# Kernel optimization log

Hardware: AMD Instinct MI355X
Metric: run time of the kernel (lower is better)

The kernel has to match this reference:

```python
import jax, jax.numpy as jnp
import numpy as np

B, S, D, H = 2, 1024, 1024, 16
DK, DV = 64, 64
E, F, K = 8, 2048, 2
FSH = 2 * F  # n_shared_experts * moe_inter_dim


def layernorm(x, w, eps=1e-8):
    # RMSNormLayer actually calls F.layer_norm(x, [dim], weight, None, eps)
    mu = jnp.mean(x, axis=-1, keepdims=True)
    var = jnp.mean((x - mu) ** 2, axis=-1, keepdims=True)
    return (x - mu) * jax.lax.rsqrt(var + eps) * w


def _forward(start_pos, x, mask, pos_embedding, attn_norm_w, ffn_norm_w,
             wq, bq, wk, bk, wv, bv, wo, bo, gate_w, gate_b,
             ew1, eb1, ew2, eb2, ew3, eb3, sw1, sb1, sw2, sb2, sw3, sb3):
    b, s, d = x.shape
    # --- attention sublayer ---
    xn = layernorm(x, attn_norm_w)
    q = (xn @ wq + bq).reshape(b, s, H, DK)
    k = (xn @ wk + bk).reshape(b, s, H, DK)
    v = (xn @ wv + bv).reshape(b, s, H, DV)
    score = jnp.einsum('bshk,bShk->bhsS', q, k) / np.float32(np.sqrt(DK))
    pe = pos_embedding[:, start_pos:start_pos + s, start_pos:start_pos + s]  # [H,s,s]
    score = score + pe[None, :, :, :] + mask[:s, :s]
    attn = jax.nn.softmax(score, axis=-1)
    o = jnp.einsum('bhsS,bShv->bshv', attn, v).reshape(b, s, H * DV)
    x = x + o @ wo + bo
    # --- MoE sublayer (eval-path math: y[t] = sum_k w[t,k]*expert_{idx[t,k]}(x[t])) ---
    hn = layernorm(x, ffn_norm_w)
    flat = hn.reshape(-1, d)  # [T, D]
    logits = flat @ gate_w.T + gate_b
    scores = jax.nn.softmax(logits, axis=-1)
    topk_w, topk_idx = jax.lax.top_k(scores, K)
    topk_w = topk_w / (jnp.sum(topk_w, axis=-1, keepdims=True) + 1e-20)
    # per-token per-expert combine weight [T, E]
    comb = jnp.sum(jax.nn.one_hot(topk_idx, E, dtype=flat.dtype) * topk_w[..., None], axis=1)
    # all experts densely (small E), SwiGLU per expert
    a = jnp.einsum('td,edf->tef', flat, ew1) + eb1
    g = jnp.einsum('td,edf->tef', flat, ew3) + eb3
    mid = jax.nn.silu(a) * g
    ye = jnp.einsum('tef,efd->ted', mid, ew2) + eb2  # [T, E, D]
    y = jnp.einsum('te,ted->td', comb, ye)
    # shared experts MLP on the normed input
    shared = (jax.nn.silu(flat @ sw1 + sb1) * (flat @ sw3 + sb3)) @ sw2 + sb2
    return x + (y + shared).reshape(b, s, d)


def setup_inputs() -> dict:
    key = jax.random.key(0)
    ks = jax.random.split(key, 16)
    def rn(i, shape, s=0.02):
        return jax.random.normal(ks[i], shape, jnp.float32) * s
    return dict(
        x=rn(0, (B, S, D), 1.0),
        start_pos=0,
        mask=jnp.zeros((S, S), jnp.float32),
        pos_embedding=rn(1, (H, S, S)),
        attn_norm_w=jnp.ones((D,), jnp.float32),
        ffn_norm_w=jnp.ones((D,), jnp.float32),
        wq=rn(2, (D, H * DK)), bq=jnp.zeros((H * DK,), jnp.float32),
        wk=rn(3, (D, H * DK)), bk=jnp.zeros((H * DK,), jnp.float32),
        wv=rn(4, (D, H * DV)), bv=jnp.zeros((H * DV,), jnp.float32),
        wo=rn(5, (H * DV, D)), bo=jnp.zeros((D,), jnp.float32),
        gate_w=rn(6, (E, D), 1.0), gate_b=rn(7, (E,), 1.0),
        ew1=rn(8, (E, D, F)), eb1=jnp.zeros((E, F), jnp.float32),
        ew2=rn(9, (E, F, D)), eb2=jnp.zeros((E, D), jnp.float32),
        ew3=rn(10, (E, D, F)), eb3=jnp.zeros((E, F), jnp.float32),
        sw1=rn(11, (D, FSH)), sb1=jnp.zeros((FSH,), jnp.float32),
        sw2=rn(12, (FSH, D)), sb2=jnp.zeros((D,), jnp.float32),
        sw3=rn(13, (D, FSH)), sb3=jnp.zeros((FSH,), jnp.float32),
    )


def reference(x, start_pos, mask, pos_embedding, attn_norm_w, ffn_norm_w,
              wq, bq, wk, bk, wv, bv, wo, bo, gate_w, gate_b,
              ew1, eb1, ew2, eb2, ew3, eb3, sw1, sb1, sw2, sb2, sw3, sb3):
    return _forward(start_pos, x, mask, pos_embedding, attn_norm_w, ffn_norm_w,
                    wq, bq, wk, bk, wv, bv, wo, bo, gate_w, gate_b,
                    ew1, eb1, ew2, eb2, ew3, eb3, sw1, sb1, sw2, sb2, sw3, sb3)
```

## Files before the change

### kernel.cpp

```cpp
#include <hip/hip_runtime.h>
#include <hip/hip_bf16.h>

#define BB 2
#define SS 1024
#define DD 1024
#define HH 16
#define DKV 64
#define EE 8
#define FF 2048
#define FSH2 4096

typedef __attribute__((ext_vector_type(8))) short bf16x8;
typedef __attribute__((ext_vector_type(4))) float f32x4;

#define EPI_PLAIN 0
#define EPI_SCATTER 2
#define AM_DENSE 0
#define AM_GATHER 1
#define AM_GROUP 2

__device__ inline unsigned pack_bf2(float lo, float hi) {
    __hip_bfloat162 h = __float22bfloat162_rn(float2{lo, hi});
    union { __hip_bfloat162 h2; unsigned u; } c; c.h2 = h; return c.u;
}
__device__ inline unsigned short bf16_1(float x) {
    union { __hip_bfloat16 b; unsigned short u; } c;
    c.b = __float2bfloat16(x); return c.u;
}

#define LOADT(s, k0) {                                                        \
    const float4* ap4 = (const float4*)(Ap + (k0));                           \
    pa##s##_0 = ap4[0]; pa##s##_1 = ap4[1];                                   \
    pa##s##_2 = ap4[2]; pa##s##_3 = ap4[3];                                   \
    const float* wp = Wcol + (size_t)((k0) + kg * 8) * N;                     \
    _Pragma("unroll")                                                         \
    for (int j = 0; j < 8; ++j) pb##s[j] = wp[(size_t)j * N];                 \
}
#define STAGET(s) {                                                           \
    uint4 aw0, aw1;                                                           \
    aw0.x = pack_bf2(pa##s##_0.x, pa##s##_0.y);                               \
    aw0.y = pack_bf2(pa##s##_0.z, pa##s##_0.w);                               \
    aw0.z = pack_bf2(pa##s##_1.x, pa##s##_1.y);                               \
    aw0.w = pack_bf2(pa##s##_1.z, pa##s##_1.w);                               \
    aw1.x = pack_bf2(pa##s##_2.x, pa##s##_2.y);                               \
    aw1.y = pack_bf2(pa##s##_2.z, pa##s##_2.w);                               \
    aw1.z = pack_bf2(pa##s##_3.x, pa##s##_3.y);                               \
    aw1.w = pack_bf2(pa##s##_3.z, pa##s##_3.w);                               \
    *(uint4*)&As[ar * 40 + ac] = aw0;                                         \
    *(uint4*)&As[ar * 40 + ac + 8] = aw1;                                     \
    uint4 bw;                                                                 \
    bw.x = pack_bf2(pb##s[0], pb##s[1]);  bw.y = pack_bf2(pb##s[2], pb##s[3]);\
    bw.z = pack_bf2(pb##s[4], pb##s[5]);  bw.w = pack_bf2(pb##s[6], pb##s[7]);\
    *(uint4*)&Bs[kg * 512 + bn * 8] = bw;                                     \
}
#define MFMAT() {                                                             \
    bf16x8 af[4], bfr[2];                                                     \
    _Pragma("unroll")                                                         \
    for (int m = 0; m < 4; ++m) {                                             \
        int row = wr * 64 + m * 16 + ll;                                      \
        af[m] = *(const bf16x8*)&As[row * 40 + lh * 8];                       \
    }                                                                         \
    _Pragma("unroll")                                                         \
    for (int n = 0; n < 2; ++n) {                                             \
        int col = wc * 32 + n * 16 + ll;                                      \
        bfr[n] = *(const bf16x8*)&Bs[lh * 512 + col * 8];                     \
    }                                                                         \
    _Pragma("unroll")                                                         \
    for (int m = 0; m < 4; ++m)                                               \
        _Pragma("unroll")                                                     \
        for (int n = 0; n < 2; ++n)                                           \
            acc[m][n] = __builtin_amdgcn_mfma_f32_16x16x32_bf16(af[m], bfr[n], acc[m][n], 0, 0, 0); \
}
#define PHASET(s, nx) {                                                       \
    STAGET(s)                                                                 \
    if ((nx) < NT) LOADT(s, (nx) << 5)                                        \
    asm volatile("s_waitcnt lgkmcnt(0)\n\ts_barrier" ::: "memory");           \
    MFMAT()                                                                   \
    asm volatile("s_barrier" ::: "memory");                                   \
}

template<int EPI, int AMODE, int NSEL, int SPLITK>
__global__ __launch_bounds__(256, 2) void mgemm(
    const float* __restrict__ A,
    const float* __restrict__ W0, const float* __restrict__ W1p, const float* __restrict__ W2p,
    const float* __restrict__ b0, const float* __restrict__ b1p, const float* __restrict__ b2p,
    const float* __restrict__ addsrc,
    float* __restrict__ C0, float* __restrict__ C1p, float* __restrict__ C2p,
    int M, int N, int K,
    const int* __restrict__ tok_list, const int* __restrict__ cnt,
    const int* __restrict__ offs, const float* __restrict__ comb,
    const int* __restrict__ idx0, float* __restrict__ y1)
{
    __shared__ __align__(16) unsigned short As[128 * 40];
    __shared__ __align__(16) unsigned short Bs[64 * 32];
    __shared__ int rows_s[128];
    const int t = threadIdx.x;
    const float* W = W0; const float* bias = b0; float* C = C0;
    if (NSEL == 3) {
        if (blockIdx.z == 1) { W = W1p; bias = b1p; C = C1p; }
        else if (blockIdx.z == 2) { W = W2p; bias = b2p; C = C2p; }
    }
    const int e = (AMODE != AM_DENSE) ? blockIdx.z : 0;
    int ne = M, base = 0;
    if (AMODE != AM_DENSE) {
        ne = cnt[e];
        base = offs[e];
        if ((int)blockIdx.y * 128 >= ne) return;
        W += (size_t)e * K * N;
        bias += (size_t)e * N;
    }
    const int m0 = blockIdx.y * 128;
    const int n0 = blockIdx.x * 64;
    if (AMODE == AM_GATHER) {
        if (t < 128) {
            int li = m0 + t; if (li >= ne) li = ne - 1;
            rows_s[t] = tok_list[e * 2048 + li];
        }
        __syncthreads();
    }
    const int ar = t >> 1;
    const int ac = (t & 1) * 16;
    const int bn = t & 63;
    const int kg = t >> 6;
    long arow;
    if (AMODE == AM_DENSE) arow = m0 + ar;
    else if (AMODE == AM_GATHER) arow = rows_s[ar];
    else { int li = m0 + ar; if (li >= ne) li = ne - 1; arow = base + li; }
    const int Kc = (SPLITK > 1) ? (K / SPLITK) : K;
    const size_t koff = (SPLITK > 1) ? (size_t)blockIdx.z * Kc : 0;
    const float* Ap = A + (size_t)arow * K + ac + koff;
    const float* Wcol = W + koff * N + n0 + bn;
    const int l = t & 63, w = t >> 6;
    const int wr = w >> 1, wc = w & 1;
    const int lh = l >> 4, ll = l & 15;
    f32x4 acc[4][2];
#pragma unroll
    for (int i = 0; i < 4; ++i)
#pragma unroll
        for (int j = 0; j < 2; ++j) acc[i][j] = f32x4{0.f, 0.f, 0.f, 0.f};

    const int NT = Kc >> 5;
    float4 pa0_0, pa0_1, pa0_2, pa0_3; float pb0[8];
    float4 pa1_0, pa1_1, pa1_2, pa1_3; float pb1[8];
    float4 pa2_0, pa2_1, pa2_2, pa2_3; float pb2[8];
    float4 pa3_0, pa3_1, pa3_2, pa3_3; float pb3[8];
    LOADT(0, 0)
    LOADT(1, 32)
    LOADT(2, 64)
    LOADT(3, 96)
    for (int it = 0; it < NT; it += 4) {
        PHASET(0, it + 4)
        PHASET(1, it + 5)
        PHASET(2, it + 6)
        PHASET(3, it + 7)
    }

#pragma unroll
    for (int m = 0; m < 4; ++m) {
#pragma unroll
        for (int n = 0; n < 2; ++n) {
            int colg = n0 + wc * 32 + n * 16 + ll;
            float bvv = (SPLITK > 1) ? 0.f : bias[colg];
#pragma unroll
            for (int j = 0; j < 4; ++j) {
                int li = m0 + wr * 64 + m * 16 + lh * 4 + j;
                float v = acc[m][n][j] + bvv;
                if (SPLITK > 1) {
                    C[(size_t)blockIdx.z * M * N + (size_t)li * N + colg] = v;
                } else if (EPI == EPI_PLAIN) {
                    if (AMODE == AM_DENSE) {
                        if (addsrc) v += addsrc[(size_t)li * N + colg];
                        C[(size_t)li * N + colg] = v;
                    } else {
                        if (li < ne) C[(size_t)(base + li) * N + colg] = v;
                    }
                } else {
                    if (li < ne) {
                        int tok = tok_list[e * 2048 + li];
                        float wgt = comb[tok * 8 + e];
                        float* dst = (idx0[tok] == e) ? C : y1;
                        dst[(size_t)tok * N + colg] = wgt * v;
                    }
                }
            }
        }
    }
}

__global__ __launch_bounds__(256, 2) void mgemmF(
    const float* __restrict__ Amid,
    const float* __restrict__ Smid,
    const float* __restrict__ W2r, const float* __restrict__ B2r,
    const float* __restrict__ W2s, const float* __restrict__ B2s,
    float* __restrict__ y0, float* __restrict__ y1, float* __restrict__ sh,
    const int* __restrict__ tok_list, const int* __restrict__ cnt,
    const int* __restrict__ offs, const float* __restrict__ comb,
    const int* __restrict__ idx0)
{
    __shared__ __align__(16) unsigned short As[128 * 40];
    __shared__ __align__(16) unsigned short Bs[64 * 32];
    const int t = threadIdx.x;
    const int z = blockIdx.z;
    const bool sh_mode = (z == 0);
    const int e = sh_mode ? 0 : (z - 1);
    const int N = DD;
    int K, ne, base;
    const float *A, *W, *bias;
    if (sh_mode) {
        K = FSH2; ne = 2048; base = 0;
        A = Smid; W = W2s; bias = B2s;
    } else {
        K = FF;
        ne = cnt[e];
        base = offs[e];
        if ((int)blockIdx.y * 128 >= ne) return;
        A = Amid;
        W = W2r + (size_t)e * K * N;
        bias = B2r + (size_t)e * N;
    }
    const int m0 = blockIdx.y * 128;
    const int n0 = blockIdx.x * 64;
    const int ar = t >> 1;
    const int ac = (t & 1) * 16;
    const int bn = t & 63;
    const int kg = t >> 6;
    long arow;
    if (sh_mode) arow = m0 + ar;
    else { int li = m0 + ar; if (li >= ne) li = ne - 1; arow = base + li; }
    const float* Ap = A + (size_t)arow * K + ac;
    const float* Wcol = W + n0 + bn;
    const int l = t & 63, w = t >> 6;
    const int wr = w >> 1, wc = w & 1;
    const int lh = l >> 4, ll = l & 15;
    f32x4 acc[4][2];
#pragma unroll
    for (int i = 0; i < 4; ++i)
#pragma unroll
        for (int j = 0; j < 2; ++j) acc[i][j] = f32x4{0.f, 0.f, 0.f, 0.f};

    const int NT = K >> 5;
    float4 pa0_0, pa0_1, pa0_2, pa0_3; float pb0[8];
    float4 pa1_0, pa1_1, pa1_2, pa1_3; float pb1[8];
    float4 pa2_0, pa2_1, pa2_2, pa2_3; float pb2[8];
    float4 pa3_0, pa3_1, pa3_2, pa3_3; float pb3[8];
    LOADT(0, 0)
    LOADT(1, 32)
    LOADT(2, 64)
    LOADT(3, 96)
    for (int it = 0; it < NT; it += 4) {
        PHASET(0, it + 4)
        PHASET(1, it + 5)
        PHASET(2, it + 6)
        PHASET(3, it + 7)
    }

#pragma unroll
    for (int m = 0; m < 4; ++m) {
#pragma unroll
        for (int n = 0; n < 2; ++n) {
            int colg = n0 + wc * 32 + n * 16 + ll;
            float bvv = bias[colg];
#pragma unroll
            for (int j = 0; j < 4; ++j) {
                int li = m0 + wr * 64 + m * 16 + lh * 4 + j;
                float v = acc[m][n][j] + bvv;
                if (sh_mode) {
                    sh[(size_t)li * N + colg] = v;
                } else {
                    if (li < ne) {
                        int tok = tok_list[e * 2048 + li];
                        float wgt = comb[tok * 8 + e];
                        float* dst = (idx0[tok] == e) ? y0 : y1;
                        dst[(size_t)tok * N + colg] = wgt * v;
                    }
                }
            }
        }
    }
}

#define LOAD2T(s, k0) {                                                       \
    const float4* ap4 = (const float4*)(Ap + (k0));                           \
    pa##s##_0 = ap4[0]; pa##s##_1 = ap4[1];                                   \
    pa##s##_2 = ap4[2]; pa##s##_3 = ap4[3];                                   \
    const float* wp1 = W1col + (size_t)((k0) + kg * 8) * N;                   \
    const float* wp3 = W3col + (size_t)((k0) + kg * 8) * N;                   \
    _Pragma("unroll")                                                         \
    for (int j = 0; j < 8; ++j) {                                             \
        pb1##s[j] = wp1[(size_t)j * N];                                       \
        pb3##s[j] = wp3[(size_t)j * N];                                       \
    }                                                                         \
}
#define STAGE2T(s) {                                                          \
    uint4 aw0, aw1;                                                           \
    aw0.x = pack_bf2(pa##s##_0.x, pa##s##_0.y);                               \
    aw0.y = pack_bf2(pa##s##_0.z, pa##s##_0.w);                               \
    aw0.z = pack_bf2(pa##s##_1.x, pa##s##_1.y);                               \
    aw0.w = pack_bf2(pa##s##_1.z, pa##s##_1.w);                               \
    aw1.x = pack_bf2(pa##s##_2.x, pa##s##_2.y);                               \
    aw1.y = pack_bf2(pa##s##_2.z, pa##s##_2.w);                               \
    aw1.z = pack_bf2(pa##s##_3.x, pa##s##_3.y);                               \
    aw1.w = pack_bf2(pa##s##_3.z, pa##s##_3.w);                               \
    *(uint4*)&As[ar * 40 + ac] = aw0;                                         \
    *(uint4*)&As[ar * 40 + ac + 8] = aw1;                                     \
    uint4 bw;                                                                 \
    bw.x = pack_bf2(pb1##s[0], pb1##s[1]);  bw.y = pack_bf2(pb1##s[2], pb1##s[3]); \
    bw.z = pack_bf2(pb1##s[4], pb1##s[5]);  bw.w = pack_bf2(pb1##s[6], pb1##s[7]); \
    *(uint4*)&B1s[kg * 512 + bn * 8] = bw;                                    \
    bw.x = pack_bf2(pb3##s[0], pb3##s[1]);  bw.y = pack_bf2(pb3##s[2], pb3##s[3]); \
    bw.z = pack_bf2(pb3##s[4], pb3##s[5]);  bw.w = pack_bf2(pb3##s[6], pb3##s[7]); \
    *(uint4*)&B3s[kg * 512 + bn * 8] = bw;                                    \
}
#define MFMA2T() {                                                            \
    bf16x8 af[4], bfr[2];                                                     \
    _Pragma("unroll")                                                         \
    for (int m = 0; m < 4; ++m) {                                             \
        int row = wr * 64 + m * 16 + ll;                                      \
        af[m] = *(const bf16x8*)&As[row * 40 + lh * 8];                       \
    }                                                                         \
    _Pragma("unroll")                                                         \
    for (int n = 0; n < 2; ++n) {                                             \
        int col = wc * 32 + n * 16 + ll;                                      \
        bfr[n] = *(const bf16x8*)&B1s[lh * 512 + col * 8];                    \
    }                                                                         \
    _Pragma("unroll")                                                         \
    for (int m = 0; m < 4; ++m)                                               \
        _Pragma("unroll")                                                     \
        for (int n = 0; n < 2; ++n)                                           \
            acc1[m][n] = __builtin_amdgcn_mfma_f32_16x16x32_bf16(af[m], bfr[n], acc1[m][n], 0, 0, 0); \
    _Pragma("unroll")                                                         \
    for (int n = 0; n < 2; ++n) {                                             \
        int col = wc * 32 + n * 16 + ll;                                      \
        bfr[n] = *(const bf16x8*)&B3s[lh * 512 + col * 8];                    \
    }                                                                         \
    _Pragma("unroll")                                                         \
    for (int m = 0; m < 4; ++m)                                               \
        _Pragma("unroll")                                                     \
        for (int n = 0; n < 2; ++n)                                           \
            acc3[m][n] = __builtin_amdgcn_mfma_f32_16x16x32_bf16(af[m], bfr[n], acc3[m][n], 0, 0, 0); \
}
#define PHASE2T(s, nx) {                                                      \
    STAGE2T(s)                                                                \
    if ((nx) < NT) LOAD2T(s, (nx) << 5)                                       \
    asm volatile("s_waitcnt lgkmcnt(0)\n\ts_barrier" ::: "memory");           \
    MFMA2T()                                                                  \
    asm volatile("s_barrier" ::: "memory");                                   \
}

#define MGEMM2_BODY(GATED) {                                                  \
    const int l = t & 63, w = t >> 6;                                         \
    const int wr = w >> 1, wc = w & 1;                                        \
    const int lh = l >> 4, ll = l & 15;                                       \
    f32x4 acc1[4][2], acc3[4][2];                                             \
    _Pragma("unroll")                                                         \
    for (int i = 0; i < 4; ++i)                                               \
        _Pragma("unroll")                                                     \
        for (int j = 0; j < 2; ++j) {                                         \
            acc1[i][j] = f32x4{0.f, 0.f, 0.f, 0.f};                           \
            acc3[i][j] = f32x4{0.f, 0.f, 0.f, 0.f};                           \
        }                                                                     \
    const int NT = K >> 5;                                                    \
    float4 pa0_0, pa0_1, pa0_2, pa0_3; float pb10[8], pb30[8];                \
    float4 pa1_0, pa1_1, pa1_2, pa1_3; float pb11[8], pb31[8];                \
    LOAD2T(0, 0)                                                              \
    LOAD2T(1, 32)                                                             \
    for (int it = 0; it < NT; it += 2) {                                      \
        PHASE2T(0, it + 2)                                                    \
        PHASE2T(1, it + 3)                                                    \
    }                                                                         \
    _Pragma("unroll")                                                         \
    for (int m = 0; m < 4; ++m) {                                             \
        _Pragma("unroll")                                                     \
        for (int n = 0; n < 2; ++n) {                                         \
            int colg = n0 + wc * 32 + n * 16 + ll;                            \
            float bv1 = b1[colg], bv3 = b3[colg];                             \
            _Pragma("unroll")                                                 \
            for (int j = 0; j < 4; ++j) {                                     \
                int li = m0 + wr * 64 + m * 16 + lh * 4 + j;                  \
                if (GATED && li >= ne) continue;                              \
                float a = acc1[m][n][j] + bv1;                                \
                float g = acc3[m][n][j] + bv3;                                \
                float sil = a / (1.0f + __expf(-a));                          \
                size_t off = (size_t)(base + li) * N + colg;                  \
                Out[off] = sil * g;                                           \
            }                                                                 \
        }                                                                     \
    }                                                                         \
}

template<int AMODE>
__global__ __launch_bounds__(256, 2) void mgemm2(
    const float* __restrict__ A,
    const float* __restrict__ W1, const float* __restrict__ W3,
    const float* __restrict__ B1, const float* __restrict__ B3,
    float* __restrict__ Out, int M, int N, int K,
    const int* __restrict__ tok_list, const int* __restrict__ cnt,
    const int* __restrict__ offs)
{
    __shared__ __align__(16) unsigned short As[128 * 40];
    __shared__ __align__(16) unsigned short B1s[64 * 32];
    __shared__ __align__(16) unsigned short B3s[64 * 32];
    __shared__ int rows_s[128];
    const int t = threadIdx.x;
    const int e = (AMODE == AM_GATHER) ? blockIdx.z : 0;
    int ne = M, base = 0;
    const float *w1 = W1, *w3 = W3, *b1 = B1, *b3 = B3;
    if (AMODE == AM_GATHER) {
        ne = cnt[e];
        base = offs[e];
        if ((int)blockIdx.y * 128 >= ne) return;
        w1 += (size_t)e * K * N; w3 += (size_t)e * K * N;
        b1 += (size_t)e * N;     b3 += (size_t)e * N;
    }
    const int m0 = blockIdx.y * 128;
    const int n0 = blockIdx.x * 64;
    if (AMODE == AM_GATHER) {
        if (t < 128) {
            int li = m0 + t; if (li >= ne) li = ne - 1;
            rows_s[t] = tok_list[e * 2048 + li];
        }
        __syncthreads();
    }
    const int ar = t >> 1;
    const int ac = (t & 1) * 16;
    const int bn = t & 63;
    const int kg = t >> 6;
    long arow = (AMODE == AM_GATHER) ? (long)rows_s[ar] : (long)(m0 + ar);
    const float* Ap = A + (size_t)arow * K + ac;
    const float* W1col = w1 + n0 + bn;
    const float* W3col = w3 + n0 + bn;
    if (AMODE == AM_GATHER) { MGEMM2_BODY(1) } else { MGEMM2_BODY(0) }
}

__global__ __launch_bounds__(256, 2) void mgemm2m(
    const float* __restrict__ A,
    const float* __restrict__ W1r, const float* __restrict__ W3r,
    const float* __restrict__ B1r, const float* __restrict__ B3r,
    const float* __restrict__ W1sh, const float* __restrict__ W3sh,
    const float* __restrict__ B1sh, const float* __restrict__ B3sh,
    float* __restrict__ OutR, float* __restrict__ OutS, int K,
    const int* __restrict__ tok_list, const int* __restrict__ cnt,
    const int* __restrict__ offs)
{
    __shared__ __align__(16) unsigned short As[128 * 40];
    __shared__ __align__(16) unsigned short B1s[64 * 32];
    __shared__ __align__(16) unsigned short B3s[64 * 32];
    __shared__ int rows_s[128];
    const int t = threadIdx.x;
    const int z = blockIdx.z;
    const bool routed = (z < 8);
    int N, ne, base;
    const float *w1, *w3, *b1, *b3;
    float* Out;
    if (routed) {
        if ((int)blockIdx.x >= FF / 64) return;
        N = FF;
        ne = cnt[z];
        base = offs[z];
        if ((int)blockIdx.y * 128 >= ne) return;
        w1 = W1r + (size_t)z * K * N; w3 = W3r + (size_t)z * K * N;
        b1 = B1r + (size_t)z * N;     b3 = B3r + (size_t)z * N;
        Out = OutR;
    } else {
        N = FSH2;
        ne = 2048;
        base = 0;
        w1 = W1sh; w3 = W3sh; b1 = B1sh; b3 = B3sh;
        Out = OutS;
    }
    const int m0 = blockIdx.y * 128;
    const int n0 = blockIdx.x * 64;
    if (routed) {
        if (t < 128) {
            int li = m0 + t; if (li >= ne) li = ne - 1;
            rows_s[t] = tok_list[z * 2048 + li];
        }
        __syncthreads();
    }
    const int ar = t >> 1;
    const int ac = (t & 1) * 16;
    const int bn = t & 63;
    const int kg = t >> 6;
    long arow = routed ? (long)rows_s[ar] : (long)(m0 + ar);
    const float* Ap = A + (size_t)arow * K + ac;
    const float* W1col = w1 + n0 + bn;
    const float* W3col = w3 + n0 + bn;
    if (routed) { MGEMM2_BODY(1) } else { MGEMM2_BODY(0) }
}

__global__ __launch_bounds__(256) void reducek(const float* __restrict__ P, int ns,
                                               const float* __restrict__ bias,
                                               const float* __restrict__ addsrc,
                                               float* __restrict__ out, int N) {
    size_t i = (size_t)blockIdx.x * 256 + threadIdx.x;
    const size_t MN4 = (size_t)2048 * N / 4;
    float4 s = ((const float4*)P)[i];
    for (int sl = 1; sl < ns; ++sl) {
        float4 p = ((const float4*)P)[i + (size_t)sl * MN4];
        s.x += p.x; s.y += p.y; s.z += p.z; s.w += p.w;
    }
    int col4 = (int)(i & ((N >> 2) - 1));
    float4 b = ((const float4*)bias)[col4];
    s.x += b.x; s.y += b.y; s.z += b.z; s.w += b.w;
    if (addsrc) {
        float4 a = ((const float4*)addsrc)[i];
        s.x += a.x; s.y += a.y; s.z += a.z; s.w += a.w;
    }
    ((float4*)out)[i] = s;
}

__global__ __launch_bounds__(256) void ln_kernel(const float* __restrict__ x,
                                                 const float* __restrict__ w,
                                                 float* __restrict__ y) {
    __shared__ float red[4], red2[4];
    const int row = blockIdx.x;
    const int t = threadIdx.x;
    const float4* xr = (const float4*)(x + (size_t)row * DD);
    float4 v = xr[t];
    float s = v.x + v.y + v.z + v.w;
    float q = v.x * v.x + v.y * v.y + v.z * v.z + v.w * v.w;
    for (int o = 32; o; o >>= 1) { s += __shfl_down(s, o); q += __shfl_down(q, o); }
    if ((t & 63) == 0) { red[t >> 6] = s; red2[t >> 6] = q; }
    __syncthreads();
    float S = red[0] + red[1] + red[2] + red[3];
    float Q = red2[0] + red2[1] + red2[2] + red2[3];
    float mu = S * (1.0f / DD);
    float var = Q * (1.0f / DD) - mu * mu;
    float inv = rsqrtf(var + 1e-8f);
    const float4* wr = (const float4*)w;
    float4 wv = wr[t];
    float4 o4;
    o4.x = (v.x - mu) * inv * wv.x;
    o4.y = (v.y - mu) * inv * wv.y;
    o4.z = (v.z - mu) * inv * wv.z;
    o4.w = (v.w - mu) * inv * wv.w;
    ((float4*)(y + (size_t)row * DD))[t] = o4;
}

__global__ __launch_bounds__(256) void attn_mfma(const float* __restrict__ Q,
                                                 const float* __restrict__ Kk,
                                                 const float* __restrict__ V,
                                                 const float* __restrict__ pe,
                                                 const float* __restrict__ mask,
                                                 const int* __restrict__ sp_ptr,
                                                 float* __restrict__ O) {
    __shared__ __align__(16) unsigned short Kt[64 * 64];
    __shared__ __align__(16) unsigned short Vt[64 * 64];
    __shared__ __align__(16) unsigned short Pl[4][16 * 64];
    const int t = threadIdx.x;
    const int w = t >> 6, l = t & 63;
    const int ll = l & 15, lh = l >> 4;
    const int bh = blockIdx.y;
    const int b = bh >> 4, h = bh & 15;
    const int q0 = blockIdx.x * 64;
    const int sp = sp_ptr[0];

    bf16x8 qf[2];
    {
        const float* qp = Q + (size_t)(b * SS + q0 + w * 16 + ll) * DD + h * 64 + lh * 8;
#pragma unroll
        for (int kk = 0; kk < 2; ++kk) {
            float4 x0 = *(const float4*)(qp + kk * 32);
            float4 x1 = *(const float4*)(qp + kk * 32 + 4);
            uint4 u;
            u.x = pack_bf2(x0.x * 0.125f, x0.y * 0.125f);
            u.y = pack_bf2(x0.z * 0.125f, x0.w * 0.125f);
            u.z = pack_bf2(x1.x * 0.125f, x1.y * 0.125f);
            u.w = pack_bf2(x1.z * 0.125f, x1.w * 0.125f);
            qf[kk] = *(bf16x8*)&u;
        }
    }
    f32x4 oacc[4];
#pragma unroll
    for (int n = 0; n < 4; ++n) oacc[n] = f32x4{0.f, 0.f, 0.f, 0.f};
    float mrun[4], lrun[4];
#pragma unroll
    for (int j = 0; j < 4; ++j) { mrun[j] = -3.0e38f; lrun[j] = 0.f; }

    const size_t pebase = (size_t)h * SS * SS + (size_t)sp;

    for (int kt0 = 0; kt0 < SS; kt0 += 64) {
        __syncthreads();
        {
            const int key = t >> 2, dg = (t & 3) * 16;
            const float* kp = Kk + (size_t)(b * SS + kt0 + key) * DD + h * 64 + dg;
            float4 k0 = *(const float4*)kp, k1 = *(const float4*)(kp + 4);
            float4 k2 = *(const float4*)(kp + 8), k3 = *(const float4*)(kp + 12);
            uint4 u0, u1;
            u0.x = pack_bf2(k0.x, k0.y); u0.y = pack_bf2(k0.z, k0.w);
            u0.z = pack_bf2(k1.x, k1.y); u0.w = pack_bf2(k1.z, k1.w);
            u1.x = pack_bf2(k2.x, k2.y); u1.y = pack_bf2(k2.z, k2.w);
            u1.z = pack_bf2(k3.x, k3.y); u1.w = pack_bf2(k3.z, k3.w);
            const int sw = (key & 7) << 4;
            *(uint4*)((char*)Kt + key * 128 + ((dg * 2) ^ sw)) = u0;
            *(uint4*)((char*)Kt + key * 128 + ((dg * 2 + 16) ^ sw)) = u1;
        }
        {
            const int kp2 = t & 31, vg = (t >> 5) * 8;
            const float* vp0 = V + (size_t)(b * SS + kt0 + 2 * kp2) * DD + h * 64 + vg;
            const float* vp1 = vp0 + DD;
            float4 a0 = *(const float4*)vp0, a1 = *(const float4*)(vp0 + 4);
            float4 b0 = *(const float4*)vp1, b1 = *(const float4*)(vp1 + 4);
            float va[8] = {a0.x, a0.y, a0.z, a0.w, a1.x, a1.y, a1.z, a1.w};
            float vb[8] = {b0.x, b0.y, b0.z, b0.w, b1.x, b1.y, b1.z, b1.w};
#pragma unroll
            for (int j = 0; j < 8; ++j) {
                int vd = vg + j;
                unsigned u = pack_bf2(va[j], vb[j]);
                *(unsigned*)((char*)Vt + vd * 128 + ((kp2 * 4) ^ ((vd & 7) << 4))) = u;
            }
        }
        __syncthreads();
        f32x4 sc[4];
#pragma unroll
        for (int n = 0; n < 4; ++n) sc[n] = f32x4{0.f, 0.f, 0.f, 0.f};
#pragma unroll
        for (int n = 0; n < 4; ++n) {
            const int key = n * 16 + ll;
            const int sw = (key & 7) << 4;
#pragma unroll
            for (int kk = 0; kk < 2; ++kk) {
                bf16x8 kf = *(const bf16x8*)((char*)Kt + key * 128 + ((kk * 64 + lh * 16) ^ sw));
                sc[n] = __builtin_amdgcn_mfma_f32_16x16x32_bf16(qf[kk], kf, sc[n], 0, 0, 0);
            }
        }
#pragma unroll
        for (int j = 0; j < 4; ++j) {
            const int qrow = q0 + w * 16 + lh * 4 + j;
            const float* per = pe + pebase + (size_t)(sp + qrow) * SS + kt0 + ll;
            const float* mar = mask + (size_t)qrow * SS + kt0 + ll;
#pragma unroll
            for (int n = 0; n < 4; ++n)
                sc[n][j] += per[n * 16] + mar[n * 16];
        }
#pragma unroll
        for (int j = 0; j < 4; ++j) {
            float mx = fmaxf(fmaxf(sc[0][j], sc[1][j]), fmaxf(sc[2][j], sc[3][j]));
#pragma unroll
            for (int o = 1; o < 16; o <<= 1) mx = fmaxf(mx, __shfl_xor(mx, o));
            float mnew = fmaxf(mrun[j], mx);
            float corr = __expf(mrun[j] - mnew);
            mrun[j] = mnew;
            float ssum = 0.f;
#pragma unroll
            for (int n = 0; n < 4; ++n) {
                float p = __expf(sc[n][j] - mnew);
                sc[n][j] = p;
                ssum += p;
            }
#pragma unroll
            for (int o = 1; o < 16; o <<= 1) ssum += __shfl_xor(ssum, o);
            lrun[j] = lrun[j] * corr + ssum;
#pragma unroll
            for (int n = 0; n < 4; ++n) oacc[n][j] *= corr;
        }
#pragma unroll
        for (int j = 0; j < 4; ++j) {
            const int lq = lh * 4 + j;
            const int sw = (lq & 7) << 4;
#pragma unroll
            for (int n = 0; n < 4; ++n) {
                const int key = n * 16 + ll;
                *(unsigned short*)((char*)Pl[w] + lq * 128 + ((key * 2) ^ sw)) =
                    bf16_1(sc[n][j]);
            }
        }
        asm volatile("s_waitcnt lgkmcnt(0)" ::: "memory");
        __builtin_amdgcn_sched_barrier(0);
#pragma unroll
        for (int kk = 0; kk < 2; ++kk) {
            const int lq = ll;
            bf16x8 pf = *(const bf16x8*)((char*)Pl[w] + lq * 128 +
                                         ((kk * 64 + lh * 16) ^ ((lq & 7) << 4)));
#pragma unroll
            for (int n = 0; n < 4; ++n) {
                const int vd = n * 16 + ll;
                bf16x8 vf = *(const bf16x8*)((char*)Vt + vd * 128 +
                                             ((kk * 64 + lh * 16) ^ ((vd & 7) << 4)));
                oacc[n] = __builtin_amdgcn_mfma_f32_16x16x32_bf16(pf, vf, oacc[n], 0, 0, 0);
            }
        }
    }
#pragma unroll
    for (int j = 0; j < 4; ++j) {
        const int qrow = q0 + w * 16 + lh * 4 + j;
        const float invl = 1.0f / lrun[j];
#pragma unroll
        for (int n = 0; n < 4; ++n)
            O[(size_t)(b * SS + qrow) * DD + h * 64 + n * 16 + ll] = oacc[n][j] * invl;
    }
}

__global__ __launch_bounds__(64) void gate_kernel(const float* __restrict__ hn,
                                                  const float* __restrict__ gw,
                                                  const float* __restrict__ gb,
                                                  float* __restrict__ comb,
                                                  int* __restrict__ idx0,
                                                  int* __restrict__ cnt,
                                                  int* __restrict__ tok_list) {
    __shared__ float lg[8];
    const int tok = blockIdx.x;
    const int lane = threadIdx.x;
    const int e = lane >> 3, chunk = lane & 7;
    const float* hr = hn + (size_t)tok * DD + chunk * 128;
    const float* gr = gw + (size_t)e * DD + chunk * 128;
    float p = 0.f;
    for (int j = 0; j < 128; ++j) p += hr[j] * gr[j];
    p += __shfl_down(p, 4, 8);
    p += __shfl_down(p, 2, 8);
    p += __shfl_down(p, 1, 8);
    if (chunk == 0) lg[e] = p + gb[e];
    __syncthreads();
    if (lane == 0) {
        float mx = lg[0];
        for (int i = 1; i < 8; ++i) mx = fmaxf(mx, lg[i]);
        float pr[8]; float ssum = 0.f;
        for (int i = 0; i < 8; ++i) { pr[i] = __expf(lg[i] - mx); ssum += pr[i]; }
        float is = 1.0f / ssum;
        for (int i = 0; i < 8; ++i) pr[i] *= is;
        int i1 = 0;
        for (int i = 1; i < 8; ++i) if (pr[i] > pr[i1]) i1 = i;
        int i2 = -1;
        for (int i = 0; i < 8; ++i) { if (i == i1) continue; if (i2 < 0 || pr[i] > pr[i2]) i2 = i; }
        float w0 = pr[i1], w1 = pr[i2];
        float nrm = 1.0f / (w0 + w1 + 1e-20f);
        w0 *= nrm; w1 *= nrm;
        for (int i = 0; i < 8; ++i) comb[tok * 8 + i] = 0.0f;
        comb[tok * 8 + i1] = w0;
        comb[tok * 8 + i2] = w1;
        idx0[tok] = i1;
        int s1 = atomicAdd(&cnt[i1], 1); tok_list[i1 * 2048 + s1] = tok;
        int s2 = atomicAdd(&cnt[i2], 1); tok_list[i2 * 2048 + s2] = tok;
    }
}

__global__ void init_cnt(int* cnt) { if (threadIdx.x < 8) cnt[threadIdx.x] = 0; }

__global__ void prefix_kernel(const int* __restrict__ cnt, int* __restrict__ offs) {
    if (threadIdx.x == 0) {
        int a = 0;
        for (int e = 0; e < 8; ++e) { offs[e] = a; a += cnt[e]; }
    }
}

__global__ __launch_bounds__(256) void final_kernel(const float* __restrict__ x2,
                                                    const float* __restrict__ y0,
                                                    const float* __restrict__ y1,
                                                    const float* __restrict__ sh,
                                                    float* __restrict__ out) {
    size_t i = (size_t)blockIdx.x * 256 + threadIdx.x;
    float4 a = ((const float4*)x2)[i];
    float4 b = ((const float4*)y0)[i];
    float4 c = ((const float4*)y1)[i];
    float4 d = ((const float4*)sh)[i];
    float4 o;
    o.x = a.x + b.x + c.x + d.x;
    o.y = a.y + b.y + c.y + d.y;
    o.z = a.z + b.z + c.z + d.z;
    o.w = a.w + b.w + c.w + d.w;
    ((float4*)out)[i] = o;
}

#define NUL6 nullptr, nullptr, nullptr, nullptr, nullptr, nullptr

extern "C" void kernel_launch(void* const* d_in, const int* in_sizes, int n_in,
                              void* d_out, int out_size, void* d_ws, size_t ws_size,
                              hipStream_t stream) {
    const float* x   = (const float*)d_in[0];
    const int*   sp  = (const int*)d_in[1];
    const float* mask= (const float*)d_in[2];
    const float* pe  = (const float*)d_in[3];
    const float* anw = (const float*)d_in[4];
    const float* fnw = (const float*)d_in[5];
    const float* wq  = (const float*)d_in[6];  const float* bq  = (const float*)d_in[7];
    const float* wk  = (const float*)d_in[8];  const float* bk  = (const float*)d_in[9];
    const float* wv  = (const float*)d_in[10]; const float* bv  = (const float*)d_in[11];
    const float* wo  = (const float*)d_in[12]; const float* bo  = (const float*)d_in[13];
    const float* gw  = (const float*)d_in[14]; const float* gb  = (const float*)d_in[15];
    const float* ew1 = (const float*)d_in[16]; const float* eb1 = (const float*)d_in[17];
    const float* ew2 = (const float*)d_in[18]; const float* eb2 = (const float*)d_in[19];
    const float* ew3 = (const float*)d_in[20]; const float* eb3 = (const float*)d_in[21];
    const float* sw1 = (const float*)d_in[22]; const float* sb1 = (const float*)d_in[23];
    const float* sw2 = (const float*)d_in[24]; const float* sb2 = (const float*)d_in[25];
    const float* sw3 = (const float*)d_in[26]; const float* sb3 = (const float*)d_in[27];

    float* ws = (float*)d_ws;
    const size_t M2 = (size_t)2048 * 1024;
    float* comb = ws;
    int* idx0   = (int*)(ws + 16384);
    int* cnt    = idx0 + 2048;
    int* offs   = cnt + 8;
    int* tok_list = offs + 8;
    float* base = ws + 65536;
    float* xn   = base;
    float* q    = base + 1 * M2;
    float* kbuf = base + 2 * M2;
    float* vbuf = base + 3 * M2;
    float* x2   = base + 4 * M2;
    float* amid = base + 5 * M2;
    float* smid = base + 9 * M2;
    const bool big = ws_size >= (size_t)(65536 + 13 * M2) * sizeof(float);
    float* o   = xn;
    float* hn  = q;
    float* y0  = xn;
    float* y1  = kbuf;
    float* sh  = vbuf;

    ln_kernel<<<2048, 256, 0, stream>>>(x, anw, xn);
    mgemm<EPI_PLAIN, AM_DENSE, 3, 1><<<dim3(16, 16, 3), 256, 0, stream>>>(
        xn, wq, wk, wv, bq, bk, bv, nullptr, q, kbuf, vbuf,
        2048, 1024, 1024, NUL6);
    attn_mfma<<<dim3(SS / 64, BB * HH), 256, 0, stream>>>(q, kbuf, vbuf, pe, mask, sp, o);
    mgemm<EPI_PLAIN, AM_DENSE, 1, 4><<<dim3(16, 16, 4), 256, 0, stream>>>(
        o, wo, nullptr, nullptr, bo, nullptr, nullptr, nullptr, amid, nullptr, nullptr,
        2048, 1024, 1024, NUL6);
    reducek<<<2048, 256, 0, stream>>>(amid, 4, bo, x, x2, 1024);
    ln_kernel<<<2048, 256, 0, stream>>>(x2, fnw, hn);
    init_cnt<<<1, 64, 0, stream>>>(cnt);
    gate_kernel<<<2048, 64, 0, stream>>>(hn, gw, gb, comb, idx0, cnt, tok_list);
    prefix_kernel<<<1, 64, 0, stream>>>(cnt, offs);

    if (big) {
        mgemm2m<<<dim3(64, 16, 9), 256, 0, stream>>>(
            hn, ew1, ew3, eb1, eb3, sw1, sw3, sb1, sb3,
            amid, smid, 1024, tok_list, cnt, offs);
        mgemmF<<<dim3(16, 16, 9), 256, 0, stream>>>(
            amid, smid, ew2, eb2, sw2, sb2, y0, y1, sh,
            tok_list, cnt, offs, comb, idx0);
    } else {
        mgemm2<AM_GATHER><<<dim3(32, 16, 8), 256, 0, stream>>>(
            hn, ew1, ew3, eb1, eb3, amid, 2048, FF, 1024, tok_list, cnt, offs);
        mgemm<EPI_SCATTER, AM_GROUP, 1, 1><<<dim3(16, 16, 8), 256, 0, stream>>>(
            amid, ew2, nullptr, nullptr, eb2, nullptr, nullptr, nullptr, y0, nullptr, nullptr,
            2048, DD, FF, tok_list, cnt, offs, comb, idx0, y1);
        mgemm2<AM_DENSE><<<dim3(64, 16), 256, 0, stream>>>(
            hn, sw1, sw3, sb1, sb3, amid, 2048, FSH2, 1024, nullptr, nullptr, nullptr);
        mgemm<EPI_PLAIN, AM_DENSE, 1, 1><<<dim3(16, 16), 256, 0, stream>>>(
            amid, sw2, nullptr, nullptr, sb2, nullptr, nullptr, nullptr, sh, nullptr, nullptr,
            2048, DD, FSH2, NUL6);
    }
    final_kernel<<<2048, 256, 0, stream>>>(x2, y0, y1, sh, (float*)d_out);
}
```

Before: 557.0 us.

## Widen fused MoE up-projection GEMM to 256-row tiles with 512 threads

Replaces the 256-thread, 128-row mgemm2m kernel with mgemm2w, which uses 512 threads and 256-row M tiles. Each half of the block loads and stages either W1 or W3, so every weight tile is shared by twice as many rows. The K loop is rewritten with two register prefetch stages, explicit barriers and a fused SiLU*gate epilogue. In exchange it uses more LDS and registers, runs one block per CU, and launches fewer, coarser blocks, which can waste work on experts with few tokens.

```diff
diff --git a/kernel.cpp b/kernel.cpp
--- a/kernel.cpp
+++ b/kernel.cpp
@@ -432,7 +432,40 @@
     if (AMODE == AM_GATHER) { MGEMM2_BODY(1) } else { MGEMM2_BODY(0) }
 }
 
-__global__ __launch_bounds__(256, 2) void mgemm2m(
+#define LOAD2W(s, k0) {                                                       \
+    const float4* ap4 = (const float4*)(Ap + (k0));                           \
+    pa##s##_0 = ap4[0]; pa##s##_1 = ap4[1];                                   \
+    pa##s##_2 = ap4[2]; pa##s##_3 = ap4[3];                                   \
+    const float* wp = Wsel + (size_t)((k0) + kg8 * 8) * N;                    \
+    _Pragma("unroll")                                                         \
+    for (int j = 0; j < 8; ++j) pbw##s[j] = wp[(size_t)j * N];                \
+}
+#define STAGE2W(s) {                                                          \
+    uint4 aw0, aw1;                                                           \
+    aw0.x = pack_bf2(pa##s##_0.x, pa##s##_0.y);                               \
+    aw0.y = pack_bf2(pa##s##_0.z, pa##s##_0.w);                               \
+    aw0.z = pack_bf2(pa##s##_1.x, pa##s##_1.y);                               \
+    aw0.w = pack_bf2(pa##s##_1.z, pa##s##_1.w);                               \
+    aw1.x = pack_bf2(pa##s##_2.x, pa##s##_2.y);                               \
+    aw1.y = pack_bf2(pa##s##_2.z, pa##s##_2.w);                               \
+    aw1.z = pack_bf2(pa##s##_3.x, pa##s##_3.y);                               \
+    aw1.w = pack_bf2(pa##s##_3.z, pa##s##_3.w);                               \
+    *(uint4*)&As[ar * 40 + ac] = aw0;                                         \
+    *(uint4*)&As[ar * 40 + ac + 8] = aw1;                                     \
+    uint4 bw;                                                                 \
+    bw.x = pack_bf2(pbw##s[0], pbw##s[1]);  bw.y = pack_bf2(pbw##s[2], pbw##s[3]); \
+    bw.z = pack_bf2(pbw##s[4], pbw##s[5]);  bw.w = pack_bf2(pbw##s[6], pbw##s[7]); \
+    *(uint4*)&Bsel[kg8 * 512 + bn * 8] = bw;                                  \
+}
+#define PHASE2W(s, nx) {                                                      \
+    STAGE2W(s)                                                                \
+    if ((nx) < NT) LOAD2W(s, (nx) << 5)                                       \
+    asm volatile("s_waitcnt lgkmcnt(0)\n\ts_barrier" ::: "memory");           \
+    MFMA2T()                                                                  \
+    asm volatile("s_barrier" ::: "memory");                                   \
+}
+
+__global__ __launch_bounds__(512, 1) void mgemm2w(
     const float* __restrict__ A,
     const float* __restrict__ W1r, const float* __restrict__ W3r,
     const float* __restrict__ B1r, const float* __restrict__ B3r,
@@ -442,10 +475,10 @@
     const int* __restrict__ tok_list, const int* __restrict__ cnt,
     const int* __restrict__ offs)
 {
-    __shared__ __align__(16) unsigned short As[128 * 40];
+    __shared__ __align__(16) unsigned short As[256 * 40];
     __shared__ __align__(16) unsigned short B1s[64 * 32];
     __shared__ __align__(16) unsigned short B3s[64 * 32];
-    __shared__ int rows_s[128];
+    __shared__ int rows_s[256];
     const int t = threadIdx.x;
     const int z = blockIdx.z;
     const bool routed = (z < 8);
@@ -457,7 +490,7 @@
         N = FF;
         ne = cnt[z];
         base = offs[z];
-        if ((int)blockIdx.y * 128 >= ne) return;
+        if ((int)blockIdx.y * 256 >= ne) return;
         w1 = W1r + (size_t)z * K * N; w3 = W3r + (size_t)z * K * N;
         b1 = B1r + (size_t)z * N;     b3 = B3r + (size_t)z * N;
         Out = OutR;
@@ -468,10 +501,10 @@
         w1 = W1sh; w3 = W3sh; b1 = B1sh; b3 = B3sh;
         Out = OutS;
     }
-    const int m0 = blockIdx.y * 128;
+    const int m0 = blockIdx.y * 256;
     const int n0 = blockIdx.x * 64;
     if (routed) {
-        if (t < 128) {
+        if (t < 256) {
             int li = m0 + t; if (li >= ne) li = ne - 1;
             rows_s[t] = tok_list[z * 2048 + li];
         }
@@ -480,12 +513,49 @@
     const int ar = t >> 1;
     const int ac = (t & 1) * 16;
     const int bn = t & 63;
-    const int kg = t >> 6;
+    const int kg8 = (t >> 6) & 3;
+    const float* Wsel = ((t < 256) ? w1 : w3) + n0 + bn;
+    unsigned short* Bsel = (t < 256) ? B1s : B3s;
     long arow = routed ? (long)rows_s[ar] : (long)(m0 + ar);
     const float* Ap = A + (size_t)arow * K + ac;
-    const float* W1col = w1 + n0 + bn;
-    const float* W3col = w3 + n0 + bn;
-    if (routed) { MGEMM2_BODY(1) } else { MGEMM2_BODY(0) }
+    const int l = t & 63, w = t >> 6;
+    const int wr = w >> 1, wc = w & 1;
+    const int lh = l >> 4, ll = l & 15;
+    f32x4 acc1[4][2], acc3[4][2];
+#pragma unroll
+    for (int i = 0; i < 4; ++i)
+#pragma unroll
+        for (int j = 0; j < 2; ++j) {
+            acc1[i][j] = f32x4{0.f, 0.f, 0.f, 0.f};
+            acc3[i][j] = f32x4{0.f, 0.f, 0.f, 0.f};
+        }
+    const int NT = K >> 5;
+    float4 pa0_0, pa0_1, pa0_2, pa0_3; float pbw0[8];
+    float4 pa1_0, pa1_1, pa1_2, pa1_3; float pbw1[8];
+    LOAD2W(0, 0)
+    LOAD2W(1, 32)
+    for (int it = 0; it < NT; it += 2) {
+        PHASE2W(0, it + 2)
+        PHASE2W(1, it + 3)
+    }
+#pragma unroll
+    for (int m = 0; m < 4; ++m) {
+#pragma unroll
+        for (int n = 0; n < 2; ++n) {
+            int colg = n0 + wc * 32 + n * 16 + ll;
+            float bv1 = b1[colg], bv3 = b3[colg];
+#pragma unroll
+            for (int j = 0; j < 4; ++j) {
+                int li = m0 + wr * 64 + m * 16 + lh * 4 + j;
+                if (routed && li >= ne) continue;
+                float a = acc1[m][n][j] + bv1;
+                float g = acc3[m][n][j] + bv3;
+                float sil = a / (1.0f + __expf(-a));
+                size_t off = (size_t)(base + li) * N + colg;
+                Out[off] = sil * g;
+            }
+        }
+    }
 }
 
 __global__ __launch_bounds__(256) void reducek(const float* __restrict__ P, int ns,
@@ -821,7 +891,7 @@
     prefix_kernel<<<1, 64, 0, stream>>>(cnt, offs);
 
     if (big) {
-        mgemm2m<<<dim3(64, 16, 9), 256, 0, stream>>>(
+        mgemm2w<<<dim3(64, 8, 9), 512, 0, stream>>>(
             hn, ew1, ew3, eb1, eb3, sw1, sw3, sb1, sb3,
             amid, smid, 1024, tok_list, cnt, offs);
         mgemmF<<<dim3(16, 16, 9), 256, 0, stream>>>(
```

Result: no change. 560.9 us (+0.7%).
